# Optimization experiments

Measured on AMD Instinct MI355X. Metric: run time of the kernel, lower is better.

## Reference

```python
import jax, jax.numpy as jnp
import numpy as np

HIDDEN = 512
ENC = 512

def setup_inputs() -> dict:
    key = jax.random.key(0)
    k1, k2, k3, k4, k5 = jax.random.split(key, 5)
    decoder_hidden = jax.random.normal(k1, (256, HIDDEN), dtype=jnp.float32)
    encoder_outputs = jax.random.normal(k2, (256, 1024, ENC), dtype=jnp.float32)
    s = 1.0 / np.sqrt(HIDDEN)
    W_h = jax.random.uniform(k3, (HIDDEN, HIDDEN), minval=-s, maxval=s, dtype=jnp.float32)
    W_s = jax.random.uniform(k4, (HIDDEN, ENC), minval=-s, maxval=s, dtype=jnp.float32)
    v = jax.random.uniform(k5, (1, HIDDEN), minval=-s, maxval=s, dtype=jnp.float32)
    return {"decoder_hidden": decoder_hidden, "encoder_outputs": encoder_outputs,
            "W_h": W_h, "W_s": W_s, "v": v}

def reference(decoder_hidden, encoder_outputs, W_h, W_s, v):
    # proj_h: (b, hidden); proj_s: (b, l, hidden)
    proj_h = decoder_hidden @ W_h.T
    proj_s = jnp.einsum('ble,he->blh', encoder_outputs, W_s)
    # additive score: v^T tanh(W_h h + W_s s_i) -> (b, l)
    scores = jnp.einsum('blh,h->bl', jnp.tanh(proj_h[:, None, :] + proj_s), v[0])
    alpha = jax.nn.softmax(scores, axis=-1)
    context = jnp.einsum('bl,ble->be', alpha, encoder_outputs)
    return (context, alpha)
```

## Files before the change

kernel.cpp:

```cpp
#include <hip/hip_runtime.h>
#include <hip/hip_bf16.h>

#define HID 512
#define ENCD 512
#define NB 256
#define SEQ 1024
#define M_TOTAL (NB * SEQ)

typedef short bf16x8 __attribute__((ext_vector_type(8)));
typedef float floatx4 __attribute__((ext_vector_type(4)));

__device__ __forceinline__ unsigned short f2bf(float f) {
    unsigned u = __builtin_bit_cast(unsigned, f);
    u += 0x7FFFu + ((u >> 16) & 1u);
    return (unsigned short)(u >> 16);
}

__global__ __launch_bounds__(256) void prep_kernel(
    const float* __restrict__ dh,
    const float* __restrict__ W_h,
    const float* __restrict__ W_s,
    float* __restrict__ proj_h,
    unsigned short* __restrict__ Ws_bf)
{
    __shared__ float sdh[HID];
    const int b = blockIdx.x;
    const int t = threadIdx.x;

    float2 d2 = ((const float2*)(dh + b * HID))[t];
    sdh[2 * t]     = d2.x;
    sdh[2 * t + 1] = d2.y;

    {
        int f4 = b * 256 + t;
        float4 w = ((const float4*)W_s)[f4];
        ushort4 o;
        o.x = f2bf(w.x); o.y = f2bf(w.y); o.z = f2bf(w.z); o.w = f2bf(w.w);
        ((ushort4*)Ws_bf)[f4] = o;
    }
    __syncthreads();

    #pragma unroll
    for (int i = 0; i < 2; ++i) {
        const int h = t + i * 256;
        const float4* wr = (const float4*)(W_h + (size_t)h * HID);
        float acc = 0.f;
        #pragma unroll 8
        for (int e4 = 0; e4 < HID / 4; ++e4) {
            float4 w = wr[e4];
            float4 s = ((const float4*)sdh)[e4];
            acc += w.x * s.x + w.y * s.y + w.z * s.z + w.w * s.w;
        }
        proj_h[b * HID + h] = acc;
    }
}

__global__ __launch_bounds__(512, 2) void score_gemm(
    const float* __restrict__ enc,
    const unsigned short* __restrict__ Ws,
    const float* __restrict__ proj_h,
    const float* __restrict__ v,
    float* __restrict__ scores)
{
    __shared__ unsigned short sA[128 * 40];
    __shared__ float sred[4][128];

    const int t    = threadIdx.x;
    const int wave = t >> 6;
    const int lane = t & 63;
    const int ln15 = lane & 15;
    const int lk   = lane >> 4;
    const int m0   = blockIdx.x * 128;
    const int bb   = m0 >> 10;
    const int wm   = (wave & 1) * 64;
    const int wn   = (wave >> 1) * 128;

    floatx4 acc[4][8] = {};

    const unsigned short* wsrow = Ws + (size_t)(wn + ln15) * HID + lk * 8;

    for (int kt = 0; kt < 16; ++kt) {
        const int k0 = kt * 32;

        bf16x8 bfrag[8];
        #pragma unroll
        for (int nj = 0; nj < 8; ++nj)
            bfrag[nj] = *(const bf16x8*)(wsrow + (size_t)nj * 16 * HID + k0);

        __syncthreads();
        #pragma unroll
        for (int i = 0; i < 2; ++i) {
            const int f  = i * 512 + t;
            const int r  = f >> 3;
            const int c4 = f & 7;
            float4 a = *(const float4*)(enc + (size_t)(m0 + r) * ENCD + k0 + c4 * 4);
            ushort4 o;
            o.x = f2bf(a.x); o.y = f2bf(a.y); o.z = f2bf(a.z); o.w = f2bf(a.w);
            *(ushort4*)(&sA[r * 40 + c4 * 4]) = o;
        }
        __syncthreads();

        #pragma unroll
        for (int mi = 0; mi < 4; ++mi) {
            bf16x8 afrag = *(const bf16x8*)(&sA[(wm + mi * 16 + ln15) * 40 + lk * 8]);
            #pragma unroll
            for (int nj = 0; nj < 8; ++nj)
                acc[mi][nj] = __builtin_amdgcn_mfma_f32_16x16x32_bf16(
                    afrag, bfrag[nj], acc[mi][nj], 0, 0, 0);
        }
    }

    float phv[8], vv[8];
    #pragma unroll
    for (int nj = 0; nj < 8; ++nj) {
        const int n = wn + nj * 16 + ln15;
        phv[nj] = proj_h[bb * HID + n];
        vv[nj]  = v[n];
    }

    #pragma unroll
    for (int mi = 0; mi < 4; ++mi) {
        #pragma unroll
        for (int r = 0; r < 4; ++r) {
            float s = 0.f;
            #pragma unroll
            for (int nj = 0; nj < 8; ++nj) {
                float x = acc[mi][nj][r] + phv[nj];
                float e = __expf(2.f * x);
                float th = 1.f - 2.f / (e + 1.f);
                s += vv[nj] * th;
            }
            s += __shfl_xor(s, 8, 64);
            s += __shfl_xor(s, 4, 64);
            s += __shfl_xor(s, 2, 64);
            s += __shfl_xor(s, 1, 64);
            if (ln15 == 0) {
                const int row = wm + mi * 16 + lk * 4 + r;
                sred[wave >> 1][row] = s;
            }
        }
    }
    __syncthreads();
    if (t < 128)
        scores[m0 + t] = sred[0][t] + sred[1][t] + sred[2][t] + sred[3][t];
}

__global__ __launch_bounds__(512) void softmax_ctx(
    const float* __restrict__ scores,
    const float* __restrict__ enc,
    float* __restrict__ ctx_out,
    float* __restrict__ alpha_out)
{
    __shared__ float salpha[SEQ];
    __shared__ float sbufA[8], sbufB[8];
    const int b = blockIdx.x;
    const int t = threadIdx.x;
    const int w = t >> 6;

    float2 sc = ((const float2*)(scores + (size_t)b * SEQ))[t];

    float mx = fmaxf(sc.x, sc.y);
    #pragma unroll
    for (int m = 32; m >= 1; m >>= 1) mx = fmaxf(mx, __shfl_xor(mx, m, 64));
    if ((t & 63) == 0) sbufA[w] = mx;
    __syncthreads();
    float gm = sbufA[0];
    #pragma unroll
    for (int i = 1; i < 8; ++i) gm = fmaxf(gm, sbufA[i]);

    float e0 = __expf(sc.x - gm);
    float e1 = __expf(sc.y - gm);
    float ssum = e0 + e1;
    #pragma unroll
    for (int m = 32; m >= 1; m >>= 1) ssum += __shfl_xor(ssum, m, 64);
    if ((t & 63) == 0) sbufB[w] = ssum;
    __syncthreads();
    float tot = 0.f;
    #pragma unroll
    for (int i = 0; i < 8; ++i) tot += sbufB[i];
    const float inv = 1.f / tot;

    const float a0 = e0 * inv, a1 = e1 * inv;
    salpha[2 * t]     = a0;
    salpha[2 * t + 1] = a1;
    ((float2*)(alpha_out + (size_t)b * SEQ))[t] = make_float2(a0, a1);
    __syncthreads();

    float acc = 0.f;
    const float* ep = enc + (size_t)b * SEQ * ENCD + t;
    #pragma unroll 8
    for (int l = 0; l < SEQ; ++l)
        acc += salpha[l] * ep[(size_t)l * ENCD];
    ctx_out[(size_t)b * ENCD + t] = acc;
}

extern "C" void kernel_launch(void* const* d_in, const int* in_sizes, int n_in,
                              void* d_out, int out_size, void* d_ws, size_t ws_size,
                              hipStream_t stream) {
    const float* dh  = (const float*)d_in[0];
    const float* enc = (const float*)d_in[1];
    const float* W_h = (const float*)d_in[2];
    const float* W_s = (const float*)d_in[3];
    const float* v   = (const float*)d_in[4];

    float* ws = (float*)d_ws;
    float* proj_h = ws;
    float* scores = ws + 131072;
    unsigned short* Ws_bf = (unsigned short*)(ws + 131072 + 262144);

    float* ctx   = (float*)d_out;
    float* alpha = (float*)d_out + NB * HID;

    prep_kernel<<<NB, 256, 0, stream>>>(dh, W_h, W_s, proj_h, Ws_bf);
    score_gemm<<<M_TOTAL / 128, 512, 0, stream>>>(enc, Ws_bf, proj_h, v, scores);
    softmax_ctx<<<NB, 512, 0, stream>>>(scores, enc, ctx, alpha);
}
```

Measured before the change: 1.084 ms.

## Load GEMM A fragments directly from global, widen softmax context and prep blocks

The score GEMM drops the shared-memory staging of the encoder tile and its two barriers per k-step. Each lane now loads its own fp32 A fragment straight from global memory, converts it to bf16 in registers, and prefetches the next k-step's fragment. The softmax/context kernel moves to 1024 threads with float4 loads over the encoder rows, split across 8 row groups and reduced in shared memory. The prep kernel handles two batch rows per block so each W_h row is reused. The trade-offs are that each encoder row tile is now loaded redundantly by the waves that share it, and register pressure rises from the prefetch buffers.

Measured after the change: 1.241 ms. 1.14x slower.

```diff
diff --git a/kernel.cpp b/kernel.cpp
--- a/kernel.cpp
+++ b/kernel.cpp
@@ -14,6 +14,15 @@
     unsigned u = __builtin_bit_cast(unsigned, f);
     u += 0x7FFFu + ((u >> 16) & 1u);
     return (unsigned short)(u >> 16);
+}
+
+__device__ __forceinline__ bf16x8 pack8(float4 a, float4 b) {
+    bf16x8 r;
+    r[0] = (short)f2bf(a.x); r[1] = (short)f2bf(a.y);
+    r[2] = (short)f2bf(a.z); r[3] = (short)f2bf(a.w);
+    r[4] = (short)f2bf(b.x); r[5] = (short)f2bf(b.y);
+    r[6] = (short)f2bf(b.z); r[7] = (short)f2bf(b.w);
+    return r;
 }
 
 __global__ __launch_bounds__(256) void prep_kernel(
@@ -23,16 +32,19 @@
     float* __restrict__ proj_h,
     unsigned short* __restrict__ Ws_bf)
 {
-    __shared__ float sdh[HID];
-    const int b = blockIdx.x;
+    __shared__ float sdh[2][HID];
+    const int blk = blockIdx.x;
     const int t = threadIdx.x;
-
-    float2 d2 = ((const float2*)(dh + b * HID))[t];
-    sdh[2 * t]     = d2.x;
-    sdh[2 * t + 1] = d2.y;
+    const int b0 = blk * 2;
 
     {
-        int f4 = b * 256 + t;
+        float4 d = ((const float4*)(dh + (size_t)b0 * HID))[t];
+        ((float4*)&sdh[0][0])[t] = d;
+    }
+
+    #pragma unroll
+    for (int i = 0; i < 2; ++i) {
+        int f4 = (blk * 256 + t) * 2 + i;
         float4 w = ((const float4*)W_s)[f4];
         ushort4 o;
         o.x = f2bf(w.x); o.y = f2bf(w.y); o.z = f2bf(w.z); o.w = f2bf(w.w);
@@ -44,14 +56,17 @@
     for (int i = 0; i < 2; ++i) {
         const int h = t + i * 256;
         const float4* wr = (const float4*)(W_h + (size_t)h * HID);
-        float acc = 0.f;
+        float acc0 = 0.f, acc1 = 0.f;
         #pragma unroll 8
         for (int e4 = 0; e4 < HID / 4; ++e4) {
-            float4 w = wr[e4];
-            float4 s = ((const float4*)sdh)[e4];
-            acc += w.x * s.x + w.y * s.y + w.z * s.z + w.w * s.w;
+            float4 w  = wr[e4];
+            float4 s0 = ((const float4*)&sdh[0][0])[e4];
+            float4 s1 = ((const float4*)&sdh[1][0])[e4];
+            acc0 += w.x * s0.x + w.y * s0.y + w.z * s0.z + w.w * s0.w;
+            acc1 += w.x * s1.x + w.y * s1.y + w.z * s1.z + w.w * s1.w;
         }
-        proj_h[b * HID + h] = acc;
+        proj_h[(size_t)b0 * HID + h]       = acc0;
+        proj_h[(size_t)(b0 + 1) * HID + h] = acc1;
     }
 }
 
@@ -62,7 +77,6 @@
     const float* __restrict__ v,
     float* __restrict__ scores)
 {
-    __shared__ unsigned short sA[128 * 40];
     __shared__ float sred[4][128];
 
     const int t    = threadIdx.x;
@@ -77,37 +91,48 @@
 
     floatx4 acc[4][8] = {};
 
-    const unsigned short* wsrow = Ws + (size_t)(wn + ln15) * HID + lk * 8;
-
+    const float* ap[4];
+    #pragma unroll
+    for (int mi = 0; mi < 4; ++mi)
+        ap[mi] = enc + (size_t)(m0 + wm + mi * 16 + ln15) * ENCD + lk * 8;
+
+    const unsigned short* bp = Ws + (size_t)(wn + ln15) * HID + lk * 8;
+
+    float4 a0[4], a1[4];
+    #pragma unroll
+    for (int mi = 0; mi < 4; ++mi) {
+        a0[mi] = *(const float4*)(ap[mi]);
+        a1[mi] = *(const float4*)(ap[mi] + 4);
+    }
+
+    #pragma unroll 2
     for (int kt = 0; kt < 16; ++kt) {
         const int k0 = kt * 32;
 
         bf16x8 bfrag[8];
         #pragma unroll
         for (int nj = 0; nj < 8; ++nj)
-            bfrag[nj] = *(const bf16x8*)(wsrow + (size_t)nj * 16 * HID + k0);
-
-        __syncthreads();
-        #pragma unroll
-        for (int i = 0; i < 2; ++i) {
-            const int f  = i * 512 + t;
-            const int r  = f >> 3;
-            const int c4 = f & 7;
-            float4 a = *(const float4*)(enc + (size_t)(m0 + r) * ENCD + k0 + c4 * 4);
-            ushort4 o;
-            o.x = f2bf(a.x); o.y = f2bf(a.y); o.z = f2bf(a.z); o.w = f2bf(a.w);
-            *(ushort4*)(&sA[r * 40 + c4 * 4]) = o;
+            bfrag[nj] = *(const bf16x8*)(bp + (size_t)nj * 16 * HID + k0);
+
+        bf16x8 afrag[4];
+        #pragma unroll
+        for (int mi = 0; mi < 4; ++mi)
+            afrag[mi] = pack8(a0[mi], a1[mi]);
+
+        if (kt < 15) {
+            #pragma unroll
+            for (int mi = 0; mi < 4; ++mi) {
+                a0[mi] = *(const float4*)(ap[mi] + k0 + 32);
+                a1[mi] = *(const float4*)(ap[mi] + k0 + 36);
+            }
         }
-        __syncthreads();
-
-        #pragma unroll
-        for (int mi = 0; mi < 4; ++mi) {
-            bf16x8 afrag = *(const bf16x8*)(&sA[(wm + mi * 16 + ln15) * 40 + lk * 8]);
+
+        #pragma unroll
+        for (int mi = 0; mi < 4; ++mi)
             #pragma unroll
             for (int nj = 0; nj < 8; ++nj)
                 acc[mi][nj] = __builtin_amdgcn_mfma_f32_16x16x32_bf16(
-                    afrag, bfrag[nj], acc[mi][nj], 0, 0, 0);
-        }
+                    afrag[mi], bfrag[nj], acc[mi][nj], 0, 0, 0);
     }
 
     float phv[8], vv[8];
@@ -145,53 +170,66 @@
         scores[m0 + t] = sred[0][t] + sred[1][t] + sred[2][t] + sred[3][t];
 }
 
-__global__ __launch_bounds__(512) void softmax_ctx(
+__global__ __launch_bounds__(1024) void softmax_ctx(
     const float* __restrict__ scores,
     const float* __restrict__ enc,
     float* __restrict__ ctx_out,
     float* __restrict__ alpha_out)
 {
     __shared__ float salpha[SEQ];
-    __shared__ float sbufA[8], sbufB[8];
+    __shared__ float sctx[8][ENCD];
+    __shared__ float sbufA[16], sbufB[16];
     const int b = blockIdx.x;
     const int t = threadIdx.x;
     const int w = t >> 6;
 
-    float2 sc = ((const float2*)(scores + (size_t)b * SEQ))[t];
-
-    float mx = fmaxf(sc.x, sc.y);
+    float sc = scores[(size_t)b * SEQ + t];
+
+    float mx = sc;
     #pragma unroll
     for (int m = 32; m >= 1; m >>= 1) mx = fmaxf(mx, __shfl_xor(mx, m, 64));
     if ((t & 63) == 0) sbufA[w] = mx;
     __syncthreads();
     float gm = sbufA[0];
     #pragma unroll
-    for (int i = 1; i < 8; ++i) gm = fmaxf(gm, sbufA[i]);
-
-    float e0 = __expf(sc.x - gm);
-    float e1 = __expf(sc.y - gm);
-    float ssum = e0 + e1;
+    for (int i = 1; i < 16; ++i) gm = fmaxf(gm, sbufA[i]);
+
+    float e0 = __expf(sc - gm);
+    float ssum = e0;
     #pragma unroll
     for (int m = 32; m >= 1; m >>= 1) ssum += __shfl_xor(ssum, m, 64);
     if ((t & 63) == 0) sbufB[w] = ssum;
     __syncthreads();
     float tot = 0.f;
     #pragma unroll
-    for (int i = 0; i < 8; ++i) tot += sbufB[i];
+    for (int i = 0; i < 16; ++i) tot += sbufB[i];
     const float inv = 1.f / tot;
 
-    const float a0 = e0 * inv, a1 = e1 * inv;
-    salpha[2 * t]     = a0;
-    salpha[2 * t + 1] = a1;
-    ((float2*)(alpha_out + (size_t)b * SEQ))[t] = make_float2(a0, a1);
-    __syncthreads();
-
-    float acc = 0.f;
-    const float* ep = enc + (size_t)b * SEQ * ENCD + t;
+    const float a0 = e0 * inv;
+    salpha[t] = a0;
+    alpha_out[(size_t)b * SEQ + t] = a0;
+    __syncthreads();
+
+    const int tx = t & 127;
+    const int ty = t >> 7;
+    float4 acc = make_float4(0.f, 0.f, 0.f, 0.f);
+    const float* ep = enc + (size_t)b * SEQ * ENCD + (size_t)tx * 4;
     #pragma unroll 8
-    for (int l = 0; l < SEQ; ++l)
-        acc += salpha[l] * ep[(size_t)l * ENCD];
-    ctx_out[(size_t)b * ENCD + t] = acc;
+    for (int l = ty; l < SEQ; l += 8) {
+        float4 vv = *(const float4*)(ep + (size_t)l * ENCD);
+        float a = salpha[l];
+        acc.x += a * vv.x; acc.y += a * vv.y;
+        acc.z += a * vv.z; acc.w += a * vv.w;
+    }
+    *(float4*)(&sctx[ty][tx * 4]) = acc;
+    __syncthreads();
+
+    if (t < ENCD) {
+        float s = 0.f;
+        #pragma unroll
+        for (int y = 0; y < 8; ++y) s += sctx[y][t];
+        ctx_out[(size_t)b * ENCD + t] = s;
+    }
 }
 
 extern "C" void kernel_launch(void* const* d_in, const int* in_sizes, int n_in,
@@ -211,7 +249,7 @@
     float* ctx   = (float*)d_out;
     float* alpha = (float*)d_out + NB * HID;
 
-    prep_kernel<<<NB, 256, 0, stream>>>(dh, W_h, W_s, proj_h, Ws_bf);
+    prep_kernel<<<128, 256, 0, stream>>>(dh, W_h, W_s, proj_h, Ws_bf);
     score_gemm<<<M_TOTAL / 128, 512, 0, stream>>>(enc, Ws_bf, proj_h, v, scores);
-    softmax_ctx<<<NB, 512, 0, stream>>>(scores, enc, ctx, alpha);
-}
+    softmax_ctx<<<NB, 1024, 0, stream>>>(scores, enc, ctx, alpha);
+}
```
